# Optimization experiments

Hardware: AMD Instinct MI355X
Metric: run time of the kernel (lower is better)

The kernel has to match this reference:

```python
import jax, jax.numpy as jnp
import numpy as np

N_HEAD = 8


def setup_inputs() -> dict:
    key = jax.random.key(0)
    ks = jax.random.split(key, 12)
    b, l, d_q, d_o, h, w = 32, 64, 1024, 512, 32, 32

    def rn(k, shape, s=0.02):
        return jax.random.normal(k, shape, jnp.float32) * s

    return {
        "q": jax.random.normal(ks[0], (b, l, d_q), jnp.float32),
        "v": jax.random.normal(ks[1], (b, d_o, h, w), jnp.float32),
        "mask": jax.random.bernoulli(ks[2], 0.2, (b, l)),
        "w_qs_w": rn(ks[3], (d_o, d_q)), "w_qs_b": jnp.zeros((d_o,), jnp.float32),
        "w_qs_att_w": rn(ks[4], (1, d_o)), "w_qs_att_b": jnp.zeros((1,), jnp.float32),
        "w_kc_w": rn(ks[5], (d_o, d_o, 1, 1)), "w_kc_b": jnp.zeros((d_o,), jnp.float32),
        "w_kd_w": rn(ks[6], (d_o, d_o, 1, 1)), "w_kd_b": jnp.zeros((d_o,), jnp.float32),
        "w_vs_w": rn(ks[7], (d_o, d_o, 1, 1)), "w_vs_b": jnp.zeros((d_o,), jnp.float32),
        "w_m_w": rn(ks[8], (1, d_o, 3, 3)), "w_m_b": jnp.zeros((1,), jnp.float32),
        "bn_gamma": jnp.ones((d_o,), jnp.float32), "bn_beta": jnp.zeros((d_o,), jnp.float32),
        "bn_mean": jnp.zeros((d_o,), jnp.float32), "bn_var": jnp.ones((d_o,), jnp.float32),
    }


def _conv1x1(x, wgt, bias):  # x: (b,c,h,w), wgt: (o,c,1,1)
    return jnp.einsum('bchw,oc->bohw', x, wgt[:, :, 0, 0]) + bias[None, :, None, None]


def reference(q, v, mask, w_qs_w, w_qs_b, w_qs_att_w, w_qs_att_b,
              w_kc_w, w_kc_b, w_kd_w, w_kd_b, w_vs_w, w_vs_b,
              w_m_w, w_m_b, bn_gamma, bn_beta, bn_mean, bn_var):
    b, l, _ = q.shape
    _, c, h, w_ = v.shape
    n = N_HEAD
    dk = c // n
    temp = float(np.power(dk, 0.5))  # sqrt(d_o // n_head)
    residual = v

    qp = q @ w_qs_w.T + w_qs_b                       # (b,l,d_o)
    flap = qp @ w_qs_att_w.T + w_qs_att_b            # (b,l,1)
    flap = jnp.where(mask[:, :, None], -1e9, flap)
    flap = jax.nn.softmax(flap, axis=-1)             # softmax over size-1 dim -> all ones (faithful to torch)

    kc = _conv1x1(v, w_kc_w, w_kc_b).reshape(b, n, dk, h * w_).transpose(0, 1, 3, 2)  # (b,n,hw,dk)
    kd = _conv1x1(v, w_kd_w, w_kd_b).reshape(b, n, dk, h * w_).transpose(0, 1, 3, 2)
    vh = _conv1x1(v, w_vs_w, w_vs_b).reshape(b, n, dk, h * w_).transpose(0, 1, 3, 2)
    qh = qp.reshape(b, l, n, dk).transpose(0, 2, 1, 3)                                 # (b,n,l,dk)

    # Collect: bmm -> weight by flap -> reduce over l -> softmax over hw -> bmm with v
    attn_col = jnp.einsum('bnld,bnsd->bnls', qh, kc)                 # (b,n,l,hw)
    attn_col = (attn_col * flap[:, None, :, :]).sum(axis=2, keepdims=True) / temp  # (b,n,1,hw)
    attn_col = jax.nn.softmax(attn_col, axis=-1)
    attn = jnp.einsum('bnus,bnsd->bnud', attn_col, vh)               # (b,n,1,dk)

    # Diffuse: bmm -> weight by flap^T -> reduce over l -> sigmoid -> outer product
    attn_dif = jnp.einsum('bnsd,bnld->bnsl', kd, qh)                 # (b,n,hw,l)
    flap_t = flap.transpose(0, 2, 1)[:, None]                        # (b,1,1,l)
    attn_dif = jax.nn.sigmoid((attn_dif * flap_t).sum(-1, keepdims=True) / temp)  # (b,n,hw,1)
    output = attn_dif * attn                                         # (b,n,hw,dk)

    # Faithful to torch permute(0,1,4,3,2).view(b,-1,h,w) (requires h==w)
    out = output.reshape(b, n, h, w_, dk).transpose(0, 1, 4, 3, 2).reshape(b, c, h, w_)
    attn_map = out

    m = jax.lax.conv_general_dilated(out, w_m_w, (1, 1), 'SAME',
                                     dimension_numbers=('NCHW', 'OIHW', 'NCHW'))
    m_attn = (m + w_m_b[None, :, None, None]).reshape(b, h * w_)

    eps = 1e-5  # BatchNorm2d eval mode
    scale = bn_gamma / jnp.sqrt(bn_var + eps)
    out = (out - bn_mean[None, :, None, None]) * scale[None, :, None, None] + bn_beta[None, :, None, None]
    out = out + residual
    out = jnp.where(out >= 0, out, 0.1 * out)  # LeakyReLU(0.1)
    return (out, m_attn, attn_map)
```

## Files before the change

kernel.cpp:

```cpp
#include <hip/hip_runtime.h>


#define BB 32
#define LL 64
#define DQn 1024
#define CCn 512
#define NH 8
#define DKn 64
#define HWn 1024
#define NBLK 512
#define SLOTSTRIDE 16

typedef unsigned short u16;
typedef unsigned int u32;
typedef unsigned long long u64;

__device__ __forceinline__ float bfr(u16 u) {
    return __uint_as_float(((u32)u) << 16);
}
__device__ __forceinline__ u16 f2bf(float f) {
    u32 x = __float_as_uint(f);
    u32 r = (x + 0x7FFFu + ((x >> 16) & 1u)) >> 16;
    return (u16)r;
}

__device__ __forceinline__ void cst(float* p, float v) {
    __hip_atomic_store(p, v, __ATOMIC_RELAXED, __HIP_MEMORY_SCOPE_AGENT);
}
__device__ __forceinline__ u32 cldu(const u32* p) {
    return __hip_atomic_load(const_cast<u32*>(p), __ATOMIC_RELAXED,
                             __HIP_MEMORY_SCOPE_AGENT);
}
__device__ __forceinline__ void cstu(u32* p, u32 v) {
    __hip_atomic_store(p, v, __ATOMIC_RELAXED, __HIP_MEMORY_SCOPE_AGENT);
}

#define POOLB 78080

struct MArgs {
    const float *q, *v, *wqs, *bqs, *wkc, *bkc, *wkd, *bkd, *wvs, *bvs, *wm, *wmb,
                *gam, *bet, *mea, *var;
    float *qsp, *qs, *wq, *bq, *dsig, *sums, *attn, *A2g, *pvp;
    u32* bar;
    float *out0, *out1, *out2;
};

__device__ __forceinline__ void gbarb(u32* slots, int b, int sc, int i) {
    u32 epoch = (u32)(i + 1);
    __syncthreads();
    int t = threadIdx.x;
    if (t < 64) {
        if (t == 0) cstu(&slots[(b * 16 + sc) * SLOTSTRIDE], epoch);
        int it = 0;
        for (;;) {
            bool ok = true;
            if (t < 16)
                ok = (cldu(&slots[(b * 16 + t) * SLOTSTRIDE]) >= epoch);
            if (__all(ok)) break;
            __builtin_amdgcn_s_sleep(1);
            if (++it > (1 << 17)) break;
        }
    }
    __syncthreads();
}

__global__ void kinit(u32* bar) {
    int t = threadIdx.x + blockIdx.x * blockDim.x;
    int total = NBLK * SLOTSTRIDE;
    for (int i = t; i < total; i += blockDim.x * gridDim.x)
        cstu(&bar[i], 0u);
}

#define PVACC(accv, eA, eB, vf) \
    accv[0] += eA.x * (vf); accv[1] += eA.y * (vf); accv[2] += eA.z * (vf); accv[3] += eA.w * (vf); \
    accv[4] += eB.x * (vf); accv[5] += eB.y * (vf); accv[6] += eB.z * (vf); accv[7] += eB.w * (vf);

__global__ void __launch_bounds__(256, 2) mega(MArgs A) {
    __builtin_amdgcn_fence(__ATOMIC_ACQUIRE, "agent");
    extern __shared__ char pool[];
    u32*   vtd = (u32*)pool;
    float* red = (float*)(pool + 65536);
    float* etb = (float*)(pool + 69888);
    float* ext = (float*)(pool + 71936);
    float* pvl   = etb;
    float* scr7  = red;
    float* al7   = red + 320;
    float* sinvp = red + 384;
    float* dsl   = red;
    float* A2l   = red + 512;
    u16*   k8s   = (u16*)etb;
    float* al    = ext;
    float* bnA   = ext + 512;
    float* bnB   = ext + 1024;

    int t = threadIdx.x;
    int bid = blockIdx.x;
    int sc = bid & 15, b = bid >> 4;
    int s0 = sc * 64;
    u32* slots = A.bar;

    {
        int dqo = t & 63, lq = t >> 6;
        const float* qp = A.q + (size_t)b * (LL * DQn) + (size_t)(lq * 16) * DQn
                        + sc * 64 + dqo;
        float acc = 0.f;
#pragma unroll
        for (int l = 0; l < 16; ++l) acc += qp[(size_t)l * DQn];
        red[dqo * 4 + lq] = acc;
    }
    __syncthreads();
    if (t < 64) {
        float a = red[t * 4] + red[t * 4 + 1] + red[t * 4 + 2] + red[t * 4 + 3];
        cst(&A.qsp[b * DQn + sc * 64 + t], a);
    }

    {
        int sp = t & 31, c2 = t >> 5;
        const float* vb = A.v + (((size_t)(b * CCn + c2 * 64)) << 10) + s0 + sp * 2;
#pragma unroll 8
        for (int cr = 0; cr < 64; ++cr) {
            int r = c2 * 64 + cr;
            float2 xv = *reinterpret_cast<const float2*>(vb + ((size_t)cr << 10));
            u32 w = (u32)f2bf(xv.x) | ((u32)f2bf(xv.y) << 16);
            vtd[r * 32 + (sp ^ (r & 31))] = w;
        }
    }
    gbarb(slots, b, sc, 0);

    {
        int dof = sc * 32 + (t >> 3);
        int part = t & 7;
        const float* qrow = A.qsp + b * DQn + part * 128;
        const float* wrow = A.wqs + (size_t)dof * DQn + part * 128;
        float acc = 0.f;
#pragma unroll 8
        for (int i = 0; i < 128; i += 4) {
            float4 qv = *reinterpret_cast<const float4*>(qrow + i);
            float4 wv = *reinterpret_cast<const float4*>(wrow + i);
            acc += wv.x * qv.x + wv.y * qv.y + wv.z * qv.z + wv.w * qv.w;
        }
        acc += __shfl_xor(acc, 4);
        acc += __shfl_xor(acc, 2);
        acc += __shfl_xor(acc, 1);
        if (part == 0) cst(&A.qs[b * CCn + dof], acc + 64.f * A.bqs[dof]);
    }
    gbarb(slots, b, sc, 1);

    {
        float2 p = *reinterpret_cast<const float2*>(&A.qs[b * CCn + t * 2]);
        etb[t * 2] = p.x; etb[t * 2 + 1] = p.y;
    }
    __syncthreads();

    if (sc == 0 && t < 16) {
        int wsel = t >> 3, n = t & 7;
        const float* bw = wsel ? A.bkd : A.bkc;
        float a2 = 0.f;
#pragma unroll 8
        for (int d = 0; d < DKn; ++d)
            a2 += etb[n * DKn + d] * bw[n * DKn + d];
        cst(&A.bq[b * 32 + wsel * 8 + n], a2);
    }

    {
        int cl = t & 31, n3 = t >> 5;
        int c = sc * 32 + cl;
#pragma unroll
        for (int wsel = 0; wsel < 2; ++wsel) {
            const float* w = wsel ? A.wkd : A.wkc;
            const float* qrow = etb + n3 * DKn;
            const float* wrow = w + (size_t)(n3 * DKn) * CCn + c;
            float acc = 0.f;
#pragma unroll 8
            for (int d = 0; d < DKn; ++d) acc += qrow[d] * wrow[(size_t)d * CCn];
            cst(&A.wq[((size_t)b * CCn + c) * 16 + wsel * 8 + n3], acc);
        }
    }
    for (int i = t; i < 64 * 17; i += 256) red[i] = 0.f;
    gbarb(slots, b, sc, 2);

    {
        float* wqL = etb;
        int s = t & 63, g2 = t >> 6;
        int sp = s >> 1, sh = (s & 1) << 4;
        float ak[16];
#pragma unroll
        for (int j = 0; j < 16; ++j) ak[j] = 0.f;
#pragma unroll 1
        for (int cc4 = 0; cc4 < 4; ++cc4) {
            __syncthreads();
            {
                const float* src = A.wq + (((size_t)b * CCn + cc4 * 128) << 4) + t * 8;
                float4 p0 = *reinterpret_cast<const float4*>(src);
                float4 p1 = *reinterpret_cast<const float4*>(src + 4);
                float* dst = wqL + t * 8;
                dst[0] = p0.x; dst[1] = p0.y; dst[2] = p0.z; dst[3] = p0.w;
                dst[4] = p1.x; dst[5] = p1.y; dst[6] = p1.z; dst[7] = p1.w;
            }
            __syncthreads();
#pragma unroll 4
            for (int i = 0; i < 32; ++i) {
                int cl = g2 * 32 + i;
                int r = cc4 * 128 + cl;
                u32 wv = vtd[r * 32 + (sp ^ (r & 31))];
                float vvf = bfr((u16)(wv >> sh));
                const float* wc = wqL + cl * 16;
#pragma unroll
                for (int j = 0; j < 16; ++j) ak[j] += wc[j] * vvf;
            }
        }
#pragma unroll
        for (int j = 0; j < 16; ++j) atomicAdd(&red[s * 17 + j], ak[j]);
    }
    __syncthreads();
    if (t < 64) {
        int s = t;
#pragma unroll
        for (int n = 0; n < NH; ++n) {
            float rc = red[s * 17 + n];
            float rd = red[s * 17 + 8 + n];
            float skc = (rc + A.bq[b * 32 + n]) * 0.125f;
            float skd = (rd + A.bq[b * 32 + 8 + n]) * 0.125f;
            etb[s * 8 + n] = __expf(skc);
            cst(&A.dsig[((size_t)(b * NH + n)) * HWn + s0 + s],
                1.f / (1.f + __expf(-skd)));
        }
    }
    __syncthreads();
    if (t < 8) {
        float a = 0.f;
#pragma unroll
        for (int s = 0; s < 64; ++s) a += etb[s * 8 + t];
        cst(&A.sums[(b * NH + t) * 16 + sc], a);
    }
    {
        float acc0[NH], acc1[NH];
#pragma unroll
        for (int n = 0; n < NH; ++n) { acc0[n] = 0.f; acc1[n] = 0.f; }
        int c0 = t, c1 = t + 256;
        int m = t & 31;
#pragma unroll 2
        for (int sp = 0; sp < 32; ++sp) {
            u32 w0 = vtd[c0 * 32 + (sp ^ m)];
            u32 w1 = vtd[c1 * 32 + (sp ^ m)];
            float va0 = bfr((u16)(w0 & 0xffffu)), va1 = bfr((u16)(w0 >> 16));
            float vb0 = bfr((u16)(w1 & 0xffffu)), vb1 = bfr((u16)(w1 >> 16));
            float4 e0a = *reinterpret_cast<const float4*>(etb + sp * 16);
            float4 e0b = *reinterpret_cast<const float4*>(etb + sp * 16 + 4);
            float4 e1a = *reinterpret_cast<const float4*>(etb + sp * 16 + 8);
            float4 e1b = *reinterpret_cast<const float4*>(etb + sp * 16 + 12);
            PVACC(acc0, e0a, e0b, va0)
            PVACC(acc0, e1a, e1b, va1)
            PVACC(acc1, e0a, e0b, vb0)
            PVACC(acc1, e1a, e1b, vb1)
        }
        size_t base = ((size_t)sc * BB + b) * NH;
#pragma unroll
        for (int n = 0; n < NH; ++n) {
            cst(&A.pvp[(base + n) * CCn + c0], acc0[n]);
            cst(&A.pvp[(base + n) * CCn + c1], acc1[n]);
        }
    }
    gbarb(slots, b, sc, 3);

    if (sc < 8) {
        int n = sc;
        for (int c = t; c < CCn; c += 256) {
            float acc = 0.f;
#pragma unroll 4
            for (int s2 = 0; s2 < 16; ++s2)
                acc += A.pvp[(((size_t)s2 * BB + b) * NH + n) * CCn + c];
            pvl[c] = acc;
        }
        if (t == 0) {
            float a = 0.f;
#pragma unroll
            for (int s2 = 0; s2 < 16; ++s2)
                a += A.sums[(b * NH + n) * 16 + s2];
            sinvp[0] = 1.f / a;
        }
        __syncthreads();
        {
            int d = t & 63, qq = t >> 6;
            const float* wrow = A.wvs + (size_t)(n * DKn + d) * CCn + qq * 128;
            const float* pq = pvl + qq * 128;
            float acc = 0.f;
#pragma unroll 4
            for (int i = 0; i < 128; ++i) acc += pq[i] * wrow[i];
            scr7[d * 5 + qq] = acc;
        }
        __syncthreads();
        if (t < 64) {
            float a = (scr7[t * 5] + scr7[t * 5 + 1] + scr7[t * 5 + 2] + scr7[t * 5 + 3])
                      * sinvp[0] + A.bvs[n * DKn + t];
            cst(&A.attn[(b * NH + n) * DKn + t], a);
            al7[t] = a;
        }
        __syncthreads();
        if (t < 9) {
            float acc = 0.f;
#pragma unroll 8
            for (int d2 = 0; d2 < DKn; ++d2)
                acc += al7[d2] * A.wm[(n * DKn + d2) * 9 + t];
            cst(&A.A2g[b * 96 + n * 9 + t], acc);
        }
    }
    gbarb(slots, b, sc, 4);

    int y0 = sc * 2;
    {
        for (int idx = t; idx < CCn; idx += 256) {
            al[idx] = A.attn[b * CCn + idx];
            float Av = A.gam[idx] * rsqrtf(A.var[idx] + 1e-5f);
            bnA[idx] = Av;
            bnB[idx] = A.bet[idx] - A.mea[idx] * Av;
        }
        for (int idx = t; idx < NH * 64; idx += 256) {
            int n = idx >> 6, r6 = idx & 63;
            int yb2 = r6 >> 5, x = r6 & 31;
            dsl[idx] = A.dsig[((size_t)(b * NH + n)) * HWn + x * 32 + y0 + yb2];
        }
        for (int idx = t; idx < 4 * NH * 32; idx += 256) {
            int ry = idx >> 8, n = (idx >> 5) & 7, x = idx & 31;
            int ycol = y0 - 1 + ry;
            float dvv = 0.f;
            if ((unsigned)ycol < 32u)
                dvv = A.dsig[((size_t)(b * NH + n)) * HWn + x * 32 + ycol];
            k8s[idx] = f2bf(dvv);
        }
        if (t < 72) A2l[t] = A.A2g[b * 96 + t];
    }
    __syncthreads();
    {
        int l = t & 63, wv = t >> 6;
        int csub = l >> 4, yb = (l >> 3) & 1, x0 = (l & 7) * 4;
        int sl = yb * 32 + x0;
#pragma unroll 2
        for (int it = 0; it < 32; ++it) {
            int c = it * 16 + wv * 4 + csub;
            int n = c >> 6;
            int m = c & 31;
            u32 w0 = vtd[c * 32 + ((sl >> 1) ^ m)];
            u32 w1 = vtd[c * 32 + (((sl >> 1) + 1) ^ m)];
            float4 dv = *reinterpret_cast<const float4*>(dsl + n * 64 + sl);
            float a = al[c], Ac = bnA[c], Bc = bnB[c];
            float p0 = a * dv.x, p1 = a * dv.y, p2 = a * dv.z, p3 = a * dv.w;
            size_t ob = (((size_t)(b * CCn + c)) << 10) + (u32)((y0 + yb) * 32 + x0);
            *reinterpret_cast<float4*>(A.out2 + ob) = make_float4(p0, p1, p2, p3);
            float o0 = fmaf(p0, Ac, Bc) + bfr((u16)(w0 & 0xffffu));
            float o1 = fmaf(p1, Ac, Bc) + bfr((u16)(w0 >> 16));
            float o2 = fmaf(p2, Ac, Bc) + bfr((u16)(w1 & 0xffffu));
            float o3 = fmaf(p3, Ac, Bc) + bfr((u16)(w1 >> 16));
            o0 = o0 < 0.f ? 0.1f * o0 : o0;
            o1 = o1 < 0.f ? 0.1f * o1 : o1;
            o2 = o2 < 0.f ? 0.1f * o2 : o2;
            o3 = o3 < 0.f ? 0.1f * o3 : o3;
            *reinterpret_cast<float4*>(A.out0 + ob) = make_float4(o0, o1, o2, o3);
        }
    }
    if (t < 64) {
        int y = y0 + (t >> 5), x = t & 31;
        float msum = 0.f;
#pragma unroll
        for (int n = 0; n < NH; ++n) {
#pragma unroll
            for (int dy = 0; dy < 3; ++dy) {
                int ry = (t >> 5) + dy;
#pragma unroll
                for (int dx = 0; dx < 3; ++dx) {
                    int xx = x + dx - 1;
                    if ((unsigned)xx < 32u)
                        msum += A2l[n * 9 + dy * 3 + dx] * bfr(k8s[ry * 256 + n * 32 + xx]);
                }
            }
        }
        A.out1[b * HWn + y * 32 + x] = msum + A.wmb[0];
    }
}


__global__ void k1_qsum_pre(const float* __restrict__ q, float* __restrict__ qsp) {
    int b = blockIdx.y;
    int dq = blockIdx.x * 256 + threadIdx.x;
    const float* qp = q + (size_t)b * LL * DQn + dq;
    float acc = 0.f;
#pragma unroll 8
    for (int l = 0; l < LL; ++l) acc += qp[l * DQn];
    qsp[b * DQn + dq] = acc;
}

__global__ void k2_qsum(const float* __restrict__ qsp, const float* __restrict__ w,
                        const float* __restrict__ bias, float* __restrict__ qs) {
    int dof = blockIdx.x;
    int t = threadIdx.x;
    int b = t & 31, ch = t >> 5;
    const float* wrow = w + (size_t)dof * DQn + ch * 128;
    const float* qrow = qsp + (size_t)b * DQn + ch * 128;
    float acc = 0.f;
#pragma unroll 8
    for (int i = 0; i < 128; i += 4) {
        float4 wv = *reinterpret_cast<const float4*>(wrow + i);
        float4 qv = *reinterpret_cast<const float4*>(qrow + i);
        acc += wv.x * qv.x + wv.y * qv.y + wv.z * qv.z + wv.w * qv.w;
    }
    __shared__ float scr[256];
    scr[t] = acc;
    __syncthreads();
    if (t < 32) {
        float a = 0.f;
#pragma unroll
        for (int c2 = 0; c2 < 8; ++c2) a += scr[c2 * 32 + t];
        qs[t * CCn + dof] = a + 64.f * bias[dof];
    }
}

__global__ void k3_wq(const float* __restrict__ qs,
                      const float* __restrict__ wkc, const float* __restrict__ bkc,
                      const float* __restrict__ wkd, const float* __restrict__ bkd,
                      float* __restrict__ wq, float* __restrict__ bq) {
    int cc = blockIdx.x, wsel = blockIdx.y, b = blockIdx.z;
    const float* w = wsel ? wkd : wkc;
    int cl = threadIdx.x & 31, n = threadIdx.x >> 5;
    int c = cc * 32 + cl;
    const float* qrow = qs + b * CCn + n * DKn;
    const float* wrow = w + (size_t)(n * DKn) * CCn + c;
    float acc = 0.f;
#pragma unroll 8
    for (int d = 0; d < DKn; ++d)
        acc += qrow[d] * wrow[(size_t)d * CCn];
    wq[((size_t)b * CCn + c) * 16 + wsel * 8 + n] = acc;
    if (cc == 0 && b == 0) {
        const float* bw = wsel ? bkd : bkc;
        int pp = threadIdx.x, bb = pp >> 3, nn = pp & 7;
        float a2 = 0.f;
#pragma unroll 8
        for (int d = 0; d < DKn; ++d)
            a2 += qs[bb * CCn + nn * DKn + d] * bw[nn * DKn + d];
        bq[wsel * 256 + pp] = a2;
    }
}

__global__ void __launch_bounds__(256) k46_scorepv(
        const float* __restrict__ v, const float* __restrict__ wq,
        const float* __restrict__ bq, float* __restrict__ dsig,
        float* __restrict__ pvp, float* __restrict__ sums) {
    int sc = blockIdx.x, b = blockIdx.y;
    __shared__ u16 vt[CCn * 33];
    __shared__ float red[4][32][17];
    __shared__ float et[32 * 8];
    int t = threadIdx.x;
    int s0 = sc * 32;
    {
        int s = t & 31, c2 = t >> 5;
        const float* vb = v + ((size_t)(b * CCn + c2 * 64) << 10) + s0 + s;
#pragma unroll 8
        for (int cr = 0; cr < 64; ++cr)
            vt[(c2 * 64 + cr) * 33 + s] = f2bf(vb[(size_t)cr << 10]);
    }
    __syncthreads();
    {
        int s = t & 31, g = t >> 5;
        float ak[16];
#pragma unroll
        for (int j = 0; j < 16; ++j) ak[j] = 0.f;
        const float* wqb = wq + ((size_t)b * CCn + g * 64) * 16;
#pragma unroll 4
        for (int i = 0; i < 64; ++i) {
            float vv = bfr(vt[(g * 64 + i) * 33 + s]);
            const float* wc = wqb + i * 16;
#pragma unroll
            for (int j = 0; j < 16; ++j) ak[j] += wc[j] * vv;
        }
#pragma unroll
        for (int j = 0; j < 16; ++j) ak[j] += __shfl_xor(ak[j], 32);
        int wv = t >> 6;
        if ((t & 63) < 32) {
#pragma unroll
            for (int j = 0; j < 16; ++j) red[wv][s][j] = ak[j];
        }
    }
    __syncthreads();
    if (t < 32) {
        int s = t;
#pragma unroll
        for (int n = 0; n < NH; ++n) {
            float rc = red[0][s][n] + red[1][s][n] + red[2][s][n] + red[3][s][n];
            float rd = red[0][s][8 + n] + red[1][s][8 + n] + red[2][s][8 + n] + red[3][s][8 + n];
            float skc = (rc + bq[b * 8 + n]) * 0.125f;
            float skd = (rd + bq[256 + b * 8 + n]) * 0.125f;
            et[s * 8 + n] = __expf(skc);
            dsig[(b * NH + n) * HWn + s0 + s] = 1.f / (1.f + __expf(-skd));
        }
    }
    __syncthreads();
    if (t < 8) {
        float a = 0.f;
#pragma unroll
        for (int s = 0; s < 32; ++s) a += et[s * 8 + t];
        sums[(b * NH + t) * 32 + sc] = a;
    }
    {
        float acc0[NH], acc1[NH];
#pragma unroll
        for (int n = 0; n < NH; ++n) { acc0[n] = 0.f; acc1[n] = 0.f; }
#pragma unroll 2
        for (int s = 0; s < 32; ++s) {
            float4 ea = *reinterpret_cast<const float4*>(et + s * 8);
            float4 eb = *reinterpret_cast<const float4*>(et + s * 8 + 4);
            float va = bfr(vt[t * 33 + s]);
            float vb2 = bfr(vt[(t + 256) * 33 + s]);
            acc0[0] += ea.x * va; acc0[1] += ea.y * va; acc0[2] += ea.z * va; acc0[3] += ea.w * va;
            acc0[4] += eb.x * va; acc0[5] += eb.y * va; acc0[6] += eb.z * va; acc0[7] += eb.w * va;
            acc1[0] += ea.x * vb2; acc1[1] += ea.y * vb2; acc1[2] += ea.z * vb2; acc1[3] += ea.w * vb2;
            acc1[4] += eb.x * vb2; acc1[5] += eb.y * vb2; acc1[6] += eb.z * vb2; acc1[7] += eb.w * vb2;
        }
        size_t base = ((size_t)sc * BB + b) * NH;
#pragma unroll
        for (int n = 0; n < NH; ++n) {
            pvp[(base + n) * CCn + t] = acc0[n];
            pvp[(base + n) * CCn + t + 256] = acc1[n];
        }
    }
}

__global__ void k7_attn(const float* __restrict__ pvp, const float* __restrict__ sums,
                        const float* __restrict__ wvs, const float* __restrict__ bvs,
                        float* __restrict__ attn) {
    int n = blockIdx.x, b = blockIdx.y;
    __shared__ float pvl[CCn];
    __shared__ float scr[64 * 5];
    __shared__ float sinv;
    int t = threadIdx.x;
    if (t == 0) {
        float a = 0.f;
#pragma unroll
        for (int sc = 0; sc < 32; ++sc) a += sums[(b * NH + n) * 32 + sc];
        sinv = 1.f / a;
    }
    for (int c = t; c < CCn; c += 256) {
        float acc = 0.f;
#pragma unroll 4
        for (int sc = 0; sc < 32; ++sc)
            acc += pvp[(((size_t)sc * BB + b) * NH + n) * CCn + c];
        pvl[c] = acc;
    }
    __syncthreads();
    int d = t & 63, qq = t >> 6;
    const float* wrow = wvs + (size_t)(n * DKn + d) * CCn + qq * 128;
    const float* pq = pvl + qq * 128;
    float acc = 0.f;
#pragma unroll 4
    for (int i = 0; i < 128; ++i) acc += pq[i] * wrow[i];
    scr[d * 5 + qq] = acc;
    __syncthreads();
    if (t < 64) {
        float a = (scr[t * 5] + scr[t * 5 + 1] + scr[t * 5 + 2] + scr[t * 5 + 3]) * sinv
                + bvs[n * DKn + t];
        attn[(b * NH + n) * DKn + t] = a;
    }
}

__global__ void k8_mattn(const float* __restrict__ dsig, const float* __restrict__ attn,
                         const float* __restrict__ wm, const float* __restrict__ wmb,
                         float* __restrict__ out1) {
    int b = blockIdx.x;
    __shared__ float dst[NH * 1056];
    __shared__ float al[CCn];
    __shared__ float A2[NH * 9];
    int t = threadIdx.x;
    al[t] = attn[b * CCn + t];
    al[t + 256] = attn[b * CCn + t + 256];
    for (int g = t; g < NH * HWn; g += 256) {
        int n = g >> 10, s = g & 1023;
        dst[n * 1056 + (s & 31) * 33 + (s >> 5)] = dsig[b * NH * HWn + g];
    }
    __syncthreads();
    if (t < 72) {
        int n = t / 9, tap = t % 9;
        float acc = 0.f;
#pragma unroll 8
        for (int d = 0; d < DKn; ++d)
            acc += al[n * DKn + d] * wm[(n * DKn + d) * 9 + tap];
        A2[t] = acc;
    }
    __syncthreads();
    float bm = wmb[0];
    for (int pos = t; pos < HWn; pos += 256) {
        int y = pos >> 5, x = pos & 31;
        float m = 0.f;
#pragma unroll
        for (int n = 0; n < NH; ++n) {
            const float* dn = dst + n * 1056;
#pragma unroll
            for (int dy = 0; dy < 3; ++dy) {
                int yy = y + dy - 1;
                if ((unsigned)yy < 32u) {
#pragma unroll
                    for (int dx = 0; dx < 3; ++dx) {
                        int xx = x + dx - 1;
                        if ((unsigned)xx < 32u)
                            m += A2[n * 9 + dy * 3 + dx] * dn[yy * 33 + xx];
                    }
                }
            }
        }
        out1[b * HWn + pos] = m + bm;
    }
}

__global__ void __launch_bounds__(256) k9_out(
        const float* __restrict__ v, const float* __restrict__ dsig,
        const float* __restrict__ attn,
        const float* __restrict__ gamma, const float* __restrict__ beta,
        const float* __restrict__ mean, const float* __restrict__ var,
        float* __restrict__ out0, float* __restrict__ out2) {
    int dh = blockIdx.x, n = blockIdx.y, b = blockIdx.z;
    __shared__ float dst[1056];
    __shared__ float al[16], bnA[16], bnB[16];
    int t = threadIdx.x;
#pragma unroll
    for (int k = 0; k < 4; ++k) {
        int s = t + k * 256;
        dst[(s & 31) * 33 + (s >> 5)] = dsig[(b * NH + n) * HWn + s];
    }
    if (t < 16) {
        int d = dh * 16 + t;
        al[t] = attn[(b * NH + n) * DKn + d];
        int ch = n * DKn + d;
        float A = gamma[ch] * rsqrtf(var[ch] + 1e-5f);
        bnA[t] = A;
        bnB[t] = beta[ch] - mean[ch] * A;
    }
    __syncthreads();
    int y = t >> 3, x = (t & 7) * 4;
    const float* dr = dst + y * 33 + x;
#pragma unroll 2
    for (int k = 0; k < 16; ++k) {
        int d = dh * 16 + k;
        size_t base = (((size_t)(b * CCn + n * DKn + d)) << 10) + y * 32 + x;
        float4 v4 = *reinterpret_cast<const float4*>(v + base);
        float a = al[k], A = bnA[k], Bc = bnB[k];
        float p0 = a * dr[0], p1 = a * dr[1], p2 = a * dr[2], p3 = a * dr[3];
        float4 mo = make_float4(p0, p1, p2, p3);
        *reinterpret_cast<float4*>(out2 + base) = mo;
        float o0 = p0 * A + Bc + v4.x;
        float o1 = p1 * A + Bc + v4.y;
        float o2 = p2 * A + Bc + v4.z;
        float o3 = p3 * A + Bc + v4.w;
        o0 = o0 < 0.f ? 0.1f * o0 : o0;
        o1 = o1 < 0.f ? 0.1f * o1 : o1;
        o2 = o2 < 0.f ? 0.1f * o2 : o2;
        o3 = o3 < 0.f ? 0.1f * o3 : o3;
        float4 oo = make_float4(o0, o1, o2, o3);
        *reinterpret_cast<float4*>(out0 + base) = oo;
    }
}

extern "C" void kernel_launch(void* const* d_in, const int* in_sizes, int n_in,
                              void* d_out, int out_size, void* d_ws, size_t ws_size,
                              hipStream_t stream) {
    (void)in_sizes; (void)n_in; (void)out_size; (void)ws_size;
    const float* q   = (const float*)d_in[0];
    const float* v   = (const float*)d_in[1];
    const float* wqs = (const float*)d_in[3];
    const float* bqs = (const float*)d_in[4];
    const float* wkc = (const float*)d_in[7];
    const float* bkc = (const float*)d_in[8];
    const float* wkd = (const float*)d_in[9];
    const float* bkd = (const float*)d_in[10];
    const float* wvs = (const float*)d_in[11];
    const float* bvs = (const float*)d_in[12];
    const float* wm  = (const float*)d_in[13];
    const float* wmb = (const float*)d_in[14];
    const float* gam = (const float*)d_in[15];
    const float* bet = (const float*)d_in[16];
    const float* mea = (const float*)d_in[17];
    const float* var = (const float*)d_in[18];

    float* ws = (float*)d_ws;
    float* out0 = (float*)d_out;
    float* out1 = out0 + 16777216;
    float* out2 = out1 + 32768;

    static int mode = -1;
    if (mode < 0) {
        hipError_t e = hipFuncSetAttribute(reinterpret_cast<const void*>(mega),
                                           hipFuncAttributeMaxDynamicSharedMemorySize,
                                           POOLB);
        mode = (e == hipSuccess) ? 1 : 0;
    }

    if (mode == 1) {
        MArgs a;
        a.q = q; a.v = v; a.wqs = wqs; a.bqs = bqs; a.wkc = wkc; a.bkc = bkc;
        a.wkd = wkd; a.bkd = bkd; a.wvs = wvs; a.bvs = bvs; a.wm = wm; a.wmb = wmb;
        a.gam = gam; a.bet = bet; a.mea = mea; a.var = var;
        a.qsp  = ws;
        a.qs   = ws + 32768;
        a.wq   = ws + 49152;
        a.bq   = ws + 311296;
        a.dsig = ws + 312320;
        a.sums = ws + 574464;
        a.attn = ws + 578560;
        a.A2g  = ws + 594944;
        a.pvp  = ws + 598016;
        a.bar  = (u32*)(ws + 2695168);
        a.out0 = out0; a.out1 = out1; a.out2 = out2;
        kinit<<<dim3(8), dim3(256), 0, stream>>>(a.bar);
        mega<<<dim3(NBLK), dim3(256), POOLB, stream>>>(a);
        return;
    }

    float* qsp  = ws + 0;
    float* qs   = ws + 32768;
    float* wq   = ws + 49152;
    float* bq   = ws + 311296;
    float* dsig = ws + 311808;
    float* sums = ws + 573952;
    float* attn = ws + 582144;
    float* pvp  = ws + 598528;

    k1_qsum_pre<<<dim3(4, 32), 256, 0, stream>>>(q, qsp);
    k2_qsum<<<dim3(512), 256, 0, stream>>>(qsp, wqs, bqs, qs);
    k3_wq<<<dim3(16, 2, 32), 256, 0, stream>>>(qs, wkc, bkc, wkd, bkd, wq, bq);
    k46_scorepv<<<dim3(32, 32), 256, 0, stream>>>(v, wq, bq, dsig, pvp, sums);
    k7_attn<<<dim3(8, 32), 256, 0, stream>>>(pvp, sums, wvs, bvs, attn);
    k8_mattn<<<dim3(32), 256, 0, stream>>>(dsig, attn, wm, wmb, out1);
    k9_out<<<dim3(4, 8, 32), 256, 0, stream>>>(v, dsig, attn, gam, bet, mea, var, out0, out2);
}
```

Baseline: 323.6 us.

## Split each batch across 32 blocks instead of 16, halving LDS per block

The persistent mega-kernel now launches 1024 blocks, 32 per batch, each owning 32 spatial positions, and halves the shared-memory pool so four blocks can be resident per CU. The per-batch software barrier now waits on 32 slots. The PV partial sums are stored as packed bf16 to cut global traffic, and the BatchNorm coefficients are computed inline instead of staged in LDS. The trade-off is more barrier participants and more partial sums to reduce, plus some precision loss in the bf16 partials.

```diff
diff --git a/kernel.cpp b/kernel.cpp
--- a/kernel.cpp
+++ b/kernel.cpp
@@ -8,12 +8,15 @@
 #define NH 8
 #define DKn 64
 #define HWn 1024
-#define NBLK 512
-#define SLOTSTRIDE 16
+#define SCN 32
+#define NBLK 1024
+#define SLOTSTRIDE 4
 
 typedef unsigned short u16;
 typedef unsigned int u32;
 typedef unsigned long long u64;
+
+#define SWZ(r) ((((r) ^ ((r) >> 4))) & 15)
 
 __device__ __forceinline__ float bfr(u16 u) {
     return __uint_as_float(((u32)u) << 16);
@@ -35,7 +38,7 @@
     __hip_atomic_store(p, v, __ATOMIC_RELAXED, __HIP_MEMORY_SCOPE_AGENT);
 }
 
-#define POOLB 78080
+#define POOLB 39040
 
 struct MArgs {
     const float *q, *v, *wqs, *bqs, *wkc, *bkc, *wkd, *bkd, *wvs, *bvs, *wm, *wmb,
@@ -50,12 +53,12 @@
     __syncthreads();
     int t = threadIdx.x;
     if (t < 64) {
-        if (t == 0) cstu(&slots[(b * 16 + sc) * SLOTSTRIDE], epoch);
+        if (t == 0) cstu(&slots[(b * 32 + sc) * SLOTSTRIDE], epoch);
         int it = 0;
         for (;;) {
             bool ok = true;
-            if (t < 16)
-                ok = (cldu(&slots[(b * 16 + t) * SLOTSTRIDE]) >= epoch);
+            if (t < 32)
+                ok = (cldu(&slots[(b * 32 + t) * SLOTSTRIDE]) >= epoch);
             if (__all(ok)) break;
             __builtin_amdgcn_s_sleep(1);
             if (++it > (1 << 17)) break;
@@ -75,70 +78,74 @@
     accv[0] += eA.x * (vf); accv[1] += eA.y * (vf); accv[2] += eA.z * (vf); accv[3] += eA.w * (vf); \
     accv[4] += eB.x * (vf); accv[5] += eB.y * (vf); accv[6] += eB.z * (vf); accv[7] += eB.w * (vf);
 
-__global__ void __launch_bounds__(256, 2) mega(MArgs A) {
+__global__ void __launch_bounds__(256, 4) mega(MArgs A) {
     __builtin_amdgcn_fence(__ATOMIC_ACQUIRE, "agent");
     extern __shared__ char pool[];
     u32*   vtd = (u32*)pool;
-    float* red = (float*)(pool + 65536);
-    float* etb = (float*)(pool + 69888);
-    float* ext = (float*)(pool + 71936);
-    float* pvl   = etb;
+    float* red = (float*)(pool + 32768);
+    float* wqr = (float*)(pool + 34944);
+    float* qsK   = wqr;
+    float* wqL   = wqr;
+    float* etb   = wqr;
+    float* pvl   = wqr;
     float* scr7  = red;
     float* al7   = red + 320;
     float* sinvp = red + 384;
-    float* dsl   = red;
-    float* A2l   = red + 512;
-    u16*   k8s   = (u16*)etb;
-    float* al    = ext;
-    float* bnA   = ext + 512;
-    float* bnB   = ext + 1024;
+    float* al    = wqr;
+    float* dsl   = wqr + 512;
+    float* A2l   = wqr + 768;
+    u16*   k8s   = (u16*)red;
 
     int t = threadIdx.x;
     int bid = blockIdx.x;
-    int sc = bid & 15, b = bid >> 4;
-    int s0 = sc * 64;
+    int sc = bid & 31, b = bid >> 5;
+    int s0 = sc * 32;
     u32* slots = A.bar;
-
-    {
-        int dqo = t & 63, lq = t >> 6;
-        const float* qp = A.q + (size_t)b * (LL * DQn) + (size_t)(lq * 16) * DQn
-                        + sc * 64 + dqo;
+    u32* pvpU = (u32*)A.pvp;
+
+    {
+        int dqo = t & 31, lq = t >> 5;
+        const float* qp = A.q + (size_t)b * (LL * DQn) + (size_t)(lq * 8) * DQn
+                        + sc * 32 + dqo;
         float acc = 0.f;
 #pragma unroll
-        for (int l = 0; l < 16; ++l) acc += qp[(size_t)l * DQn];
-        red[dqo * 4 + lq] = acc;
-    }
-    __syncthreads();
-    if (t < 64) {
-        float a = red[t * 4] + red[t * 4 + 1] + red[t * 4 + 2] + red[t * 4 + 3];
-        cst(&A.qsp[b * DQn + sc * 64 + t], a);
-    }
-
-    {
-        int sp = t & 31, c2 = t >> 5;
-        const float* vb = A.v + (((size_t)(b * CCn + c2 * 64)) << 10) + s0 + sp * 2;
-#pragma unroll 8
-        for (int cr = 0; cr < 64; ++cr) {
-            int r = c2 * 64 + cr;
+        for (int l = 0; l < 8; ++l) acc += qp[(size_t)l * DQn];
+        red[lq * 32 + dqo] = acc;
+    }
+    __syncthreads();
+    if (t < 32) {
+        float a = 0.f;
+#pragma unroll
+        for (int k = 0; k < 8; ++k) a += red[k * 32 + t];
+        cst(&A.qsp[b * DQn + sc * 32 + t], a);
+    }
+
+    {
+        int sp = t & 15, c2 = t >> 4;
+        const float* vb = A.v + (((size_t)(b * CCn + c2 * 32)) << 10) + s0 + sp * 2;
+#pragma unroll 8
+        for (int cr = 0; cr < 32; ++cr) {
+            int r = c2 * 32 + cr;
             float2 xv = *reinterpret_cast<const float2*>(vb + ((size_t)cr << 10));
             u32 w = (u32)f2bf(xv.x) | ((u32)f2bf(xv.y) << 16);
-            vtd[r * 32 + (sp ^ (r & 31))] = w;
+            vtd[r * 16 + (sp ^ SWZ(r))] = w;
         }
     }
     gbarb(slots, b, sc, 0);
 
     {
-        int dof = sc * 32 + (t >> 3);
-        int part = t & 7;
-        const float* qrow = A.qsp + b * DQn + part * 128;
-        const float* wrow = A.wqs + (size_t)dof * DQn + part * 128;
+        int dof = sc * 16 + (t >> 4);
+        int part = t & 15;
+        const float* qrow = A.qsp + b * DQn + part * 64;
+        const float* wrow = A.wqs + (size_t)dof * DQn + part * 64;
         float acc = 0.f;
 #pragma unroll 8
-        for (int i = 0; i < 128; i += 4) {
+        for (int i = 0; i < 64; i += 4) {
             float4 qv = *reinterpret_cast<const float4*>(qrow + i);
             float4 wv = *reinterpret_cast<const float4*>(wrow + i);
             acc += wv.x * qv.x + wv.y * qv.y + wv.z * qv.z + wv.w * qv.w;
         }
+        acc += __shfl_xor(acc, 8);
         acc += __shfl_xor(acc, 4);
         acc += __shfl_xor(acc, 2);
         acc += __shfl_xor(acc, 1);
@@ -148,7 +155,7 @@
 
     {
         float2 p = *reinterpret_cast<const float2*>(&A.qs[b * CCn + t * 2]);
-        etb[t * 2] = p.x; etb[t * 2 + 1] = p.y;
+        qsK[t * 2] = p.x; qsK[t * 2 + 1] = p.y;
     }
     __syncthreads();
 
@@ -158,62 +165,57 @@
         float a2 = 0.f;
 #pragma unroll 8
         for (int d = 0; d < DKn; ++d)
-            a2 += etb[n * DKn + d] * bw[n * DKn + d];
+            a2 += qsK[n * DKn + d] * bw[n * DKn + d];
         cst(&A.bq[b * 32 + wsel * 8 + n], a2);
     }
 
     {
-        int cl = t & 31, n3 = t >> 5;
-        int c = sc * 32 + cl;
-#pragma unroll
-        for (int wsel = 0; wsel < 2; ++wsel) {
-            const float* w = wsel ? A.wkd : A.wkc;
-            const float* qrow = etb + n3 * DKn;
-            const float* wrow = w + (size_t)(n3 * DKn) * CCn + c;
-            float acc = 0.f;
-#pragma unroll 8
-            for (int d = 0; d < DKn; ++d) acc += qrow[d] * wrow[(size_t)d * CCn];
-            cst(&A.wq[((size_t)b * CCn + c) * 16 + wsel * 8 + n3], acc);
-        }
-    }
-    for (int i = t; i < 64 * 17; i += 256) red[i] = 0.f;
+        int cl = t & 15, n3 = (t >> 4) & 7, wsel = t >> 7;
+        int c = sc * 16 + cl;
+        const float* w = wsel ? A.wkd : A.wkc;
+        const float* qrow = qsK + n3 * DKn;
+        const float* wrow = w + (size_t)(n3 * DKn) * CCn + c;
+        float acc = 0.f;
+#pragma unroll 8
+        for (int d = 0; d < DKn; ++d) acc += qrow[d] * wrow[(size_t)d * CCn];
+        cst(&A.wq[((size_t)b * CCn + c) * 16 + wsel * 8 + n3], acc);
+    }
+    __syncthreads();
+    for (int i = t; i < 544; i += 256) red[i] = 0.f;
     gbarb(slots, b, sc, 2);
 
     {
-        float* wqL = etb;
-        int s = t & 63, g2 = t >> 6;
+        int s = t & 31, g = t >> 5;
         int sp = s >> 1, sh = (s & 1) << 4;
         float ak[16];
 #pragma unroll
         for (int j = 0; j < 16; ++j) ak[j] = 0.f;
 #pragma unroll 1
-        for (int cc4 = 0; cc4 < 4; ++cc4) {
+        for (int cc8 = 0; cc8 < 8; ++cc8) {
             __syncthreads();
             {
-                const float* src = A.wq + (((size_t)b * CCn + cc4 * 128) << 4) + t * 8;
-                float4 p0 = *reinterpret_cast<const float4*>(src);
-                float4 p1 = *reinterpret_cast<const float4*>(src + 4);
-                float* dst = wqL + t * 8;
-                dst[0] = p0.x; dst[1] = p0.y; dst[2] = p0.z; dst[3] = p0.w;
-                dst[4] = p1.x; dst[5] = p1.y; dst[6] = p1.z; dst[7] = p1.w;
+                const float* src = A.wq + (((size_t)b * CCn + cc8 * 64) << 4) + t * 4;
+                float4 p = *reinterpret_cast<const float4*>(src);
+                *reinterpret_cast<float4*>(wqL + t * 4) = p;
             }
             __syncthreads();
-#pragma unroll 4
-            for (int i = 0; i < 32; ++i) {
-                int cl = g2 * 32 + i;
-                int r = cc4 * 128 + cl;
-                u32 wv = vtd[r * 32 + (sp ^ (r & 31))];
+#pragma unroll
+            for (int i = 0; i < 8; ++i) {
+                int cl = g * 8 + i;
+                int r = cc8 * 64 + cl;
+                u32 wv = vtd[r * 16 + (sp ^ SWZ(r))];
                 float vvf = bfr((u16)(wv >> sh));
                 const float* wc = wqL + cl * 16;
 #pragma unroll
                 for (int j = 0; j < 16; ++j) ak[j] += wc[j] * vvf;
             }
         }
+        __syncthreads();
 #pragma unroll
         for (int j = 0; j < 16; ++j) atomicAdd(&red[s * 17 + j], ak[j]);
     }
     __syncthreads();
-    if (t < 64) {
+    if (t < 32) {
         int s = t;
 #pragma unroll
         for (int n = 0; n < NH; ++n) {
@@ -230,19 +232,19 @@
     if (t < 8) {
         float a = 0.f;
 #pragma unroll
-        for (int s = 0; s < 64; ++s) a += etb[s * 8 + t];
-        cst(&A.sums[(b * NH + t) * 16 + sc], a);
+        for (int s = 0; s < 32; ++s) a += etb[s * 8 + t];
+        cst(&A.sums[(b * NH + t) * 32 + sc], a);
     }
     {
         float acc0[NH], acc1[NH];
 #pragma unroll
         for (int n = 0; n < NH; ++n) { acc0[n] = 0.f; acc1[n] = 0.f; }
         int c0 = t, c1 = t + 256;
-        int m = t & 31;
+        int sw0 = SWZ(c0), sw1 = SWZ(c1);
 #pragma unroll 2
-        for (int sp = 0; sp < 32; ++sp) {
-            u32 w0 = vtd[c0 * 32 + (sp ^ m)];
-            u32 w1 = vtd[c1 * 32 + (sp ^ m)];
+        for (int sp = 0; sp < 16; ++sp) {
+            u32 w0 = vtd[c0 * 16 + (sp ^ sw0)];
+            u32 w1 = vtd[c1 * 16 + (sp ^ sw1)];
             float va0 = bfr((u16)(w0 & 0xffffu)), va1 = bfr((u16)(w0 >> 16));
             float vb0 = bfr((u16)(w1 & 0xffffu)), vb1 = bfr((u16)(w1 >> 16));
             float4 e0a = *reinterpret_cast<const float4*>(etb + sp * 16);
@@ -254,29 +256,32 @@
             PVACC(acc1, e0a, e0b, vb0)
             PVACC(acc1, e1a, e1b, vb1)
         }
-        size_t base = ((size_t)sc * BB + b) * NH;
+        size_t base = ((size_t)(sc * BB + b)) * NH;
 #pragma unroll
         for (int n = 0; n < NH; ++n) {
-            cst(&A.pvp[(base + n) * CCn + c0], acc0[n]);
-            cst(&A.pvp[(base + n) * CCn + c1], acc1[n]);
+            u32 pk = (u32)f2bf(acc0[n]) | ((u32)f2bf(acc1[n]) << 16);
+            cstu(&pvpU[(base + n) * 256 + t], pk);
         }
     }
     gbarb(slots, b, sc, 3);
 
     if (sc < 8) {
         int n = sc;
-        for (int c = t; c < CCn; c += 256) {
-            float acc = 0.f;
+        {
+            float a0 = 0.f, a1 = 0.f;
 #pragma unroll 4
-            for (int s2 = 0; s2 < 16; ++s2)
-                acc += A.pvp[(((size_t)s2 * BB + b) * NH + n) * CCn + c];
-            pvl[c] = acc;
+            for (int s2 = 0; s2 < 32; ++s2) {
+                u32 pw = pvpU[(((size_t)(s2 * BB + b)) * NH + n) * 256 + t];
+                a0 += bfr((u16)(pw & 0xffffu));
+                a1 += bfr((u16)(pw >> 16));
+            }
+            pvl[t] = a0; pvl[t + 256] = a1;
         }
         if (t == 0) {
             float a = 0.f;
 #pragma unroll
-            for (int s2 = 0; s2 < 16; ++s2)
-                a += A.sums[(b * NH + n) * 16 + s2];
+            for (int s2 = 0; s2 < 32; ++s2)
+                a += A.sums[(b * NH + n) * 32 + s2];
             sinvp[0] = 1.f / a;
         }
         __syncthreads();
@@ -307,22 +312,17 @@
     }
     gbarb(slots, b, sc, 4);
 
-    int y0 = sc * 2;
-    {
-        for (int idx = t; idx < CCn; idx += 256) {
+    int y = sc;
+    {
+        for (int idx = t; idx < CCn; idx += 256)
             al[idx] = A.attn[b * CCn + idx];
-            float Av = A.gam[idx] * rsqrtf(A.var[idx] + 1e-5f);
-            bnA[idx] = Av;
-            bnB[idx] = A.bet[idx] - A.mea[idx] * Av;
-        }
-        for (int idx = t; idx < NH * 64; idx += 256) {
-            int n = idx >> 6, r6 = idx & 63;
-            int yb2 = r6 >> 5, x = r6 & 31;
-            dsl[idx] = A.dsig[((size_t)(b * NH + n)) * HWn + x * 32 + y0 + yb2];
-        }
-        for (int idx = t; idx < 4 * NH * 32; idx += 256) {
+        if (t < 256) {
+            int n = t >> 5, x = t & 31;
+            dsl[t] = A.dsig[((size_t)(b * NH + n)) * HWn + x * 32 + y];
+        }
+        for (int idx = t; idx < 768; idx += 256) {
             int ry = idx >> 8, n = (idx >> 5) & 7, x = idx & 31;
-            int ycol = y0 - 1 + ry;
+            int ycol = y - 1 + ry;
             float dvv = 0.f;
             if ((unsigned)ycol < 32u)
                 dvv = A.dsig[((size_t)(b * NH + n)) * HWn + x * 32 + ycol];
@@ -332,20 +332,21 @@
     }
     __syncthreads();
     {
-        int l = t & 63, wv = t >> 6;
-        int csub = l >> 4, yb = (l >> 3) & 1, x0 = (l & 7) * 4;
-        int sl = yb * 32 + x0;
+        int xq = t & 7, cb = t >> 3;
+        int x0 = xq * 4;
 #pragma unroll 2
-        for (int it = 0; it < 32; ++it) {
-            int c = it * 16 + wv * 4 + csub;
+        for (int k = 0; k < 16; ++k) {
+            int c = cb + (k << 5);
             int n = c >> 6;
-            int m = c & 31;
-            u32 w0 = vtd[c * 32 + ((sl >> 1) ^ m)];
-            u32 w1 = vtd[c * 32 + (((sl >> 1) + 1) ^ m)];
-            float4 dv = *reinterpret_cast<const float4*>(dsl + n * 64 + sl);
-            float a = al[c], Ac = bnA[c], Bc = bnB[c];
+            float a = al[c];
+            float Ac = A.gam[c] * rsqrtf(A.var[c] + 1e-5f);
+            float Bc = A.bet[c] - A.mea[c] * Ac;
+            int sw = SWZ(c);
+            u32 w0 = vtd[c * 16 + ((x0 >> 1) ^ sw)];
+            u32 w1 = vtd[c * 16 + (((x0 >> 1) + 1) ^ sw)];
+            float4 dv = *reinterpret_cast<const float4*>(dsl + n * 32 + x0);
             float p0 = a * dv.x, p1 = a * dv.y, p2 = a * dv.z, p3 = a * dv.w;
-            size_t ob = (((size_t)(b * CCn + c)) << 10) + (u32)((y0 + yb) * 32 + x0);
+            size_t ob = (((size_t)(b * CCn + c)) << 10) + (u32)((y << 5) + x0);
             *reinterpret_cast<float4*>(A.out2 + ob) = make_float4(p0, p1, p2, p3);
             float o0 = fmaf(p0, Ac, Bc) + bfr((u16)(w0 & 0xffffu));
             float o1 = fmaf(p1, Ac, Bc) + bfr((u16)(w0 >> 16));
@@ -358,19 +359,18 @@
             *reinterpret_cast<float4*>(A.out0 + ob) = make_float4(o0, o1, o2, o3);
         }
     }
-    if (t < 64) {
-        int y = y0 + (t >> 5), x = t & 31;
+    if (t < 32) {
+        int x = t;
         float msum = 0.f;
 #pragma unroll
         for (int n = 0; n < NH; ++n) {
 #pragma unroll
             for (int dy = 0; dy < 3; ++dy) {
-                int ry = (t >> 5) + dy;
 #pragma unroll
                 for (int dx = 0; dx < 3; ++dx) {
                     int xx = x + dx - 1;
                     if ((unsigned)xx < 32u)
-                        msum += A2l[n * 9 + dy * 3 + dx] * bfr(k8s[ry * 256 + n * 32 + xx]);
+                        msum += A2l[n * 9 + dy * 3 + dx] * bfr(k8s[dy * 256 + n * 32 + xx]);
                 }
             }
         }
@@ -701,12 +701,12 @@
         a.bq   = ws + 311296;
         a.dsig = ws + 312320;
         a.sums = ws + 574464;
-        a.attn = ws + 578560;
-        a.A2g  = ws + 594944;
-        a.pvp  = ws + 598016;
-        a.bar  = (u32*)(ws + 2695168);
+        a.attn = ws + 582656;
+        a.A2g  = ws + 599040;
+        a.pvp  = ws + 602112;
+        a.bar  = (u32*)(ws + 2699264);
         a.out0 = out0; a.out1 = out1; a.out2 = out2;
-        kinit<<<dim3(8), dim3(256), 0, stream>>>(a.bar);
+        kinit<<<dim3(4), dim3(256), 0, stream>>>(a.bar);
         mega<<<dim3(NBLK), dim3(256), POOLB, stream>>>(a);
         return;
     }
```

After: 347.3 us. 7.3% more time.
